# Optimization experiments

Measured on AMD Instinct MI355X. Metric: run time of the kernel, lower is better.

Reference implementation:

```python
import jax, jax.numpy as jnp
import numpy as np

N, D, F1, F2, F3, H = 4096, 512, 64, 32, 16, 4
ALPHA = 0.2  # LeakyReLU negative slope
NEG = -9e15


def setup_inputs() -> dict:
    key = jax.random.key(0)
    ks = jax.random.split(key, 11)
    # sparse binary adjacency with self loops (adj.to_dense() in original)
    adj = (jax.random.uniform(ks[1], (N, N)) < 0.01).astype(jnp.float32)
    adj = jnp.maximum(adj, jnp.eye(N, dtype=jnp.float32))
    return {
        "x": jax.random.normal(ks[0], (N, D), jnp.float32),
        "adj": adj,
        "W_heads": jax.random.normal(ks[2], (H, D, F1), jnp.float32) * 0.05,
        "a_heads": jax.random.normal(ks[3], (H, 2 * F1, 1), jnp.float32) * 0.05,
        "W_att": jax.random.normal(ks[4], (H * F1, F1), jnp.float32) * 0.05,
        "a_att": jax.random.normal(ks[5], (2 * F1, 1), jnp.float32) * 0.05,
        "W1": jax.random.normal(ks[6], (F1, F2), jnp.float32) * 0.05,
        "W2": jax.random.normal(ks[7], (F2, F3), jnp.float32) * 0.05,
        "W3": jax.random.normal(ks[8], (F2, F3), jnp.float32) * 0.05,
        "eps": jax.random.normal(ks[9], (N, F3), jnp.float32),
    }


def _gat(x, adj, W, a, out_dim):
    Wh = x @ W                                   # [N, F]
    e = (Wh @ a[:out_dim]) + (Wh @ a[out_dim:]).T  # [N,1] + [1,N] -> [N,N]
    e = jax.nn.leaky_relu(e, negative_slope=ALPHA)
    att = jax.nn.softmax(jnp.where(adj > 0, e, NEG), axis=-1)
    return jax.nn.elu(att @ Wh)                  # [N, F]


def reference(x, adj, W_heads, a_heads, W_att, a_att, W1, W2, W3, eps):
    # multi-head GAT, concat along feature dim
    heads = jax.vmap(lambda W, a: _gat(x, adj, W, a, F1))(W_heads, a_heads)  # [H,N,F1]
    cat = jnp.transpose(heads, (1, 0, 2)).reshape(N, H * F1)
    gc_att = _gat(cat, adj, W_att, a_att, F1)    # [N, F1]
    # GCN layers (dropout off, no bias): spmm(adj, x @ W)
    h1 = jax.nn.relu(adj @ (gc_att @ W1))        # [N, F2]
    mu = adj @ (h1 @ W2)                         # [N, F3]
    logvar = adj @ (h1 @ W3)                     # [N, F3]
    # reparameterize (vae_bool=True): eps * exp(logvar) + mu
    z = eps * jnp.exp(logvar) + mu
    adj_rec = z @ z.T                            # inner-product decoder [N,N]
    return adj_rec, mu, logvar
```

## Files before the change

kernel.cpp:

```cpp
#include <hip/hip_runtime.h>
#include <math.h>

#define NN 4096
#define DD 512
#define F1 64
#define F2 32
#define F3 16
#define NH 4
#define ALPHA 0.2f
#define CAP 160

__device__ __forceinline__ float lrelu(float e) { return (e >= 0.f) ? e : ALPHA * e; }

__global__ void k_csr(const float* __restrict__ adj, int* __restrict__ colidx,
                      int* __restrict__ deg) {
  __shared__ int cnt;
  int i = blockIdx.x, tid = threadIdx.x;
  if (tid == 0) cnt = 0;
  __syncthreads();
  const float4* arow = (const float4*)(adj + (size_t)i * NN);
  for (int t = tid; t < NN / 4; t += 256) {
    float4 v = arow[t];
    int base = t * 4;
    if (v.x != 0.f) { int p = atomicAdd(&cnt, 1); if (p < CAP) colidx[(size_t)i * CAP + p] = base; }
    if (v.y != 0.f) { int p = atomicAdd(&cnt, 1); if (p < CAP) colidx[(size_t)i * CAP + p] = base + 1; }
    if (v.z != 0.f) { int p = atomicAdd(&cnt, 1); if (p < CAP) colidx[(size_t)i * CAP + p] = base + 2; }
    if (v.w != 0.f) { int p = atomicAdd(&cnt, 1); if (p < CAP) colidx[(size_t)i * CAP + p] = base + 3; }
  }
  __syncthreads();
  if (tid == 0) deg[i] = cnt < CAP ? cnt : CAP;
}

__global__ __launch_bounds__(256) void k_wh_gemm(
    const float* __restrict__ x, const float* __restrict__ W_heads,
    const float* __restrict__ a_heads, float* __restrict__ Whcat,
    float* __restrict__ s1, float* __restrict__ s2) {
  __shared__ float As[2][32][65];
  __shared__ float Bs[2][32][64];
  int tid = threadIdx.x;
  int h = blockIdx.y;
  int r0 = blockIdx.x * 64;
  const float* Wh = W_heads + (size_t)h * DD * F1;

  int sr = tid >> 3, sq = tid & 7;
  int bk = tid >> 4, bf = tid & 15;
  int rg = tid >> 4, cg = tid & 15;

  const float* xa0 = x + (size_t)(r0 + sr) * DD;
  const float* xa1 = x + (size_t)(r0 + sr + 32) * DD;

  float4 pa0 = *(const float4*)(xa0 + sq * 4);
  float4 pa1 = *(const float4*)(xa1 + sq * 4);
  float4 pb0 = *(const float4*)(Wh + (size_t)bk * F1 + bf * 4);
  float4 pb1 = *(const float4*)(Wh + (size_t)(bk + 16) * F1 + bf * 4);
  {
    float* a0p = &As[0][sq * 4][sr];
    a0p[0] = pa0.x; a0p[65] = pa0.y; a0p[130] = pa0.z; a0p[195] = pa0.w;
    float* a1p = &As[0][sq * 4][sr + 32];
    a1p[0] = pa1.x; a1p[65] = pa1.y; a1p[130] = pa1.z; a1p[195] = pa1.w;
    *(float4*)&Bs[0][bk][bf * 4] = pb0;
    *(float4*)&Bs[0][bk + 16][bf * 4] = pb1;
  }
  __syncthreads();

  float acc[4][4] = {};
  for (int c = 0; c < 16; ++c) {
    int cb = c & 1;
    if (c < 15) {
      int k0 = (c + 1) * 32;
      pa0 = *(const float4*)(xa0 + k0 + sq * 4);
      pa1 = *(const float4*)(xa1 + k0 + sq * 4);
      pb0 = *(const float4*)(Wh + (size_t)(k0 + bk) * F1 + bf * 4);
      pb1 = *(const float4*)(Wh + (size_t)(k0 + bk + 16) * F1 + bf * 4);
    }
#pragma unroll
    for (int kk = 0; kk < 32; ++kk) {
      float4 av = *(const float4*)&As[cb][kk][rg * 4];
      float4 bv = *(const float4*)&Bs[cb][kk][cg * 4];
      acc[0][0] = fmaf(av.x, bv.x, acc[0][0]);
      acc[0][1] = fmaf(av.x, bv.y, acc[0][1]);
      acc[0][2] = fmaf(av.x, bv.z, acc[0][2]);
      acc[0][3] = fmaf(av.x, bv.w, acc[0][3]);
      acc[1][0] = fmaf(av.y, bv.x, acc[1][0]);
      acc[1][1] = fmaf(av.y, bv.y, acc[1][1]);
      acc[1][2] = fmaf(av.y, bv.z, acc[1][2]);
      acc[1][3] = fmaf(av.y, bv.w, acc[1][3]);
      acc[2][0] = fmaf(av.z, bv.x, acc[2][0]);
      acc[2][1] = fmaf(av.z, bv.y, acc[2][1]);
      acc[2][2] = fmaf(av.z, bv.z, acc[2][2]);
      acc[2][3] = fmaf(av.z, bv.w, acc[2][3]);
      acc[3][0] = fmaf(av.w, bv.x, acc[3][0]);
      acc[3][1] = fmaf(av.w, bv.y, acc[3][1]);
      acc[3][2] = fmaf(av.w, bv.z, acc[3][2]);
      acc[3][3] = fmaf(av.w, bv.w, acc[3][3]);
    }
    if (c < 15) {
      int nb = cb ^ 1;
      float* a0p = &As[nb][sq * 4][sr];
      a0p[0] = pa0.x; a0p[65] = pa0.y; a0p[130] = pa0.z; a0p[195] = pa0.w;
      float* a1p = &As[nb][sq * 4][sr + 32];
      a1p[0] = pa1.x; a1p[65] = pa1.y; a1p[130] = pa1.z; a1p[195] = pa1.w;
      *(float4*)&Bs[nb][bk][bf * 4] = pb0;
      *(float4*)&Bs[nb][bk + 16][bf * 4] = pb1;
      __syncthreads();
    }
  }

  float4 a1v = *(const float4*)&a_heads[h * 2 * F1 + cg * 4];
  float4 a2v = *(const float4*)&a_heads[h * 2 * F1 + F1 + cg * 4];
#pragma unroll
  for (int r = 0; r < 4; ++r) {
    int row = r0 + rg * 4 + r;
    *(float4*)&Whcat[(size_t)row * (NH * F1) + h * 64 + cg * 4] =
        make_float4(acc[r][0], acc[r][1], acc[r][2], acc[r][3]);
    float v1 = acc[r][0] * a1v.x + acc[r][1] * a1v.y + acc[r][2] * a1v.z + acc[r][3] * a1v.w;
    float v2 = acc[r][0] * a2v.x + acc[r][1] * a2v.y + acc[r][2] * a2v.z + acc[r][3] * a2v.w;
#pragma unroll
    for (int off = 8; off > 0; off >>= 1) {
      v1 += __shfl_down(v1, off, 16);
      v2 += __shfl_down(v2, off, 16);
    }
    if (cg == 0) {
      s1[h * NN + row] = v1;
      s2[h * NN + row] = v2;
    }
  }
}

__global__ void k_gat_heads(const int* __restrict__ colidx, const int* __restrict__ deg,
                            const float* __restrict__ Whcat,
                            const float* __restrict__ s1, const float* __restrict__ s2,
                            float* __restrict__ cat) {
  __shared__ int idx[CAP];
  __shared__ float wsh[NH][CAP];
  int i = blockIdx.x, tid = threadIdx.x;
  int c = deg[i];
  for (int t = tid; t < c; t += 256) idx[t] = colidx[(size_t)i * CAP + t];
  __syncthreads();
  int h = tid >> 6;
  int f = tid & 63;
  const float* s2h = s2 + h * NN;
  float s1v = s1[h * NN + i];
  float M = -INFINITY;
  for (int k = f; k < c; k += 64) {
    float v = s2h[idx[k]];
    wsh[h][k] = v;
    M = fmaxf(M, v);
  }
#pragma unroll
  for (int off = 32; off > 0; off >>= 1) M = fmaxf(M, __shfl_down(M, off, 64));
  M = __shfl(M, 0, 64);
  float m = lrelu(s1v + M);
  float lsum = 0.f;
  for (int k = f; k < c; k += 64) {
    float w = __expf(lrelu(s1v + wsh[h][k]) - m);
    wsh[h][k] = w;
    lsum += w;
  }
#pragma unroll
  for (int off = 32; off > 0; off >>= 1) lsum += __shfl_down(lsum, off, 64);
  float linv = 1.f / __shfl(lsum, 0, 64);
  __syncthreads();
  const float* base = Whcat + h * 64 + f;
  float a0 = 0.f, a1 = 0.f, a2 = 0.f, a3 = 0.f;
  int k = 0;
  for (; k + 4 <= c; k += 4) {
    int j0 = idx[k], j1 = idx[k + 1], j2 = idx[k + 2], j3 = idx[k + 3];
    a0 = fmaf(wsh[h][k],     base[(size_t)j0 * 256], a0);
    a1 = fmaf(wsh[h][k + 1], base[(size_t)j1 * 256], a1);
    a2 = fmaf(wsh[h][k + 2], base[(size_t)j2 * 256], a2);
    a3 = fmaf(wsh[h][k + 3], base[(size_t)j3 * 256], a3);
  }
  for (; k < c; ++k) a0 = fmaf(wsh[h][k], base[(size_t)idx[k] * 256], a0);
  float o = (a0 + a1 + a2 + a3) * linv;
  cat[(size_t)i * (NH * F1) + tid] = (o > 0.f) ? o : expm1f(o);
}

__global__ void k_wh2(const float* __restrict__ cat,
                      const float* __restrict__ W_att,
                      const float* __restrict__ a_att,
                      float* __restrict__ Wh2,
                      float* __restrict__ s1b, float* __restrict__ s2b) {
  const int ROWS = 8;
  __shared__ float cs[ROWS][NH * F1];
  int tid = threadIdx.x;
  int r0 = blockIdx.x * ROWS;
  const float4* csrc = (const float4*)(cat + (size_t)r0 * 256);
  for (int t = tid; t < ROWS * 256 / 4; t += 256) ((float4*)cs)[t] = csrc[t];
  __syncthreads();
  int g = tid >> 6;
  int f = tid & 63;
  float a1 = a_att[f], a2 = a_att[64 + f];
  const float* W = W_att + f;
#pragma unroll
  for (int rr = 0; rr < 2; ++rr) {
    int r = g * 2 + rr;
    float acc = 0.f;
    for (int k = 0; k < 256; k += 4) {
      float4 cv = *(const float4*)&cs[r][k];
      acc = fmaf(cv.x, W[(k + 0) * 64], acc);
      acc = fmaf(cv.y, W[(k + 1) * 64], acc);
      acc = fmaf(cv.z, W[(k + 2) * 64], acc);
      acc = fmaf(cv.w, W[(k + 3) * 64], acc);
    }
    Wh2[(size_t)(r0 + r) * 64 + f] = acc;
    float v1 = acc * a1, v2 = acc * a2;
#pragma unroll
    for (int off = 32; off > 0; off >>= 1) {
      v1 += __shfl_down(v1, off, 64);
      v2 += __shfl_down(v2, off, 64);
    }
    if (f == 0) { s1b[r0 + r] = v1; s2b[r0 + r] = v2; }
  }
}

__global__ void k_gat2t1(const int* __restrict__ colidx, const int* __restrict__ deg,
                         const float* __restrict__ Wh2,
                         const float* __restrict__ s1b, const float* __restrict__ s2b,
                         const float* __restrict__ W1, float* __restrict__ t1) {
  __shared__ int idx4[4][CAP];
  __shared__ float wsh4[4][CAP];
  __shared__ float grow[4][64];
  __shared__ float W1s[F1 * F2];
  int tid = threadIdx.x;
  int w = tid >> 6, f = tid & 63;
  int i = blockIdx.x * 4 + w;
  int c = deg[i];
  for (int t = tid; t < F1 * F2; t += 256) W1s[t] = W1[t];
  for (int k = f; k < c; k += 64) idx4[w][k] = colidx[(size_t)i * CAP + k];
  __syncthreads();
  float s1v = s1b[i];
  float M = -INFINITY;
  for (int k = f; k < c; k += 64) {
    float v = s2b[idx4[w][k]];
    wsh4[w][k] = v;
    M = fmaxf(M, v);
  }
#pragma unroll
  for (int off = 32; off > 0; off >>= 1) M = fmaxf(M, __shfl_down(M, off, 64));
  M = __shfl(M, 0, 64);
  float m = lrelu(s1v + M);
  float lsum = 0.f;
  for (int k = f; k < c; k += 64) {
    float wv = __expf(lrelu(s1v + wsh4[w][k]) - m);
    wsh4[w][k] = wv;
    lsum += wv;
  }
#pragma unroll
  for (int off = 32; off > 0; off >>= 1) lsum += __shfl_down(lsum, off, 64);
  float linv = 1.f / __shfl(lsum, 0, 64);
  __syncthreads();
  const float* base = Wh2 + f;
  float a0 = 0.f, a1 = 0.f, a2 = 0.f, a3 = 0.f;
  int k = 0;
  for (; k + 4 <= c; k += 4) {
    int j0 = idx4[w][k], j1 = idx4[w][k + 1], j2 = idx4[w][k + 2], j3 = idx4[w][k + 3];
    a0 = fmaf(wsh4[w][k],     base[(size_t)j0 * 64], a0);
    a1 = fmaf(wsh4[w][k + 1], base[(size_t)j1 * 64], a1);
    a2 = fmaf(wsh4[w][k + 2], base[(size_t)j2 * 64], a2);
    a3 = fmaf(wsh4[w][k + 3], base[(size_t)j3 * 64], a3);
  }
  for (; k < c; ++k) a0 = fmaf(wsh4[w][k], base[(size_t)idx4[w][k] * 64], a0);
  float o = (a0 + a1 + a2 + a3) * linv;
  grow[w][f] = (o > 0.f) ? o : expm1f(o);
  __syncthreads();
  if (f < F2) {
    float acc = 0.f;
#pragma unroll 8
    for (int kk = 0; kk < F1; ++kk) acc = fmaf(grow[w][kk], W1s[kk * F2 + f], acc);
    t1[(size_t)i * F2 + f] = acc;
  }
}

__global__ void k_gcn1t23(const int* __restrict__ colidx, const int* __restrict__ deg,
                          const float* __restrict__ t1,
                          const float* __restrict__ W2, const float* __restrict__ W3,
                          float* __restrict__ t23) {
  __shared__ int idx4[4][CAP];
  __shared__ float hrow[4][F2];
  __shared__ float Wc[F2 * 32];
  int tid = threadIdx.x;
  int w = tid >> 6, lane = tid & 63;
  int nb = lane >> 5, g = lane & 31;
  int i = blockIdx.x * 4 + w;
  int c = deg[i];
  for (int t = tid; t < F2 * 32; t += 256) {
    int kk = t >> 5, gg = t & 31;
    Wc[t] = (gg < 16) ? W2[kk * 16 + gg] : W3[kk * 16 + (gg - 16)];
  }
  for (int k = lane; k < c; k += 64) idx4[w][k] = colidx[(size_t)i * CAP + k];
  __syncthreads();
  float a0 = 0.f, a1 = 0.f;
  int k = nb;
  for (; k + 2 < c; k += 4) {
    a0 += t1[(size_t)idx4[w][k] * F2 + g];
    a1 += t1[(size_t)idx4[w][k + 2] * F2 + g];
  }
  for (; k < c; k += 2) a0 += t1[(size_t)idx4[w][k] * F2 + g];
  float tot = a0 + a1;
  tot += __shfl_xor(tot, 32, 64);
  float h1v = fmaxf(tot, 0.f);
  if (nb == 0) hrow[w][g] = h1v;
  __syncthreads();
  if (lane < 32) {
    float acc = 0.f;
#pragma unroll 8
    for (int kk = 0; kk < F2; ++kk) acc = fmaf(hrow[w][kk], Wc[kk * 32 + lane], acc);
    t23[(size_t)i * 32 + lane] = acc;
  }
}

__global__ void k_gcn2(const int* __restrict__ colidx, const int* __restrict__ deg,
                       const float* __restrict__ t23, const float* __restrict__ eps,
                       float* __restrict__ mu_out, float* __restrict__ lv_out,
                       float* __restrict__ z) {
  __shared__ int idx4[4][CAP];
  int tid = threadIdx.x;
  int w = tid >> 6, lane = tid & 63;
  int nb = lane >> 5, g = lane & 31;
  int i = blockIdx.x * 4 + w;
  int c = deg[i];
  for (int k = lane; k < c; k += 64) idx4[w][k] = colidx[(size_t)i * CAP + k];
  __syncthreads();
  float a0 = 0.f, a1 = 0.f;
  int k = nb;
  for (; k + 2 < c; k += 4) {
    a0 += t23[(size_t)idx4[w][k] * 32 + g];
    a1 += t23[(size_t)idx4[w][k + 2] * 32 + g];
  }
  for (; k < c; k += 2) a0 += t23[(size_t)idx4[w][k] * 32 + g];
  float tot = a0 + a1;
  tot += __shfl_xor(tot, 32, 64);
  float lvv = __shfl(tot, (lane & 31) + 16, 64);
  if (lane < 16) {
    mu_out[(size_t)i * 16 + g] = tot;
    z[(size_t)i * 16 + g] = eps[(size_t)i * 16 + g] * expf(lvv) + tot;
  } else if (lane < 32) {
    lv_out[(size_t)i * 16 + (g - 16)] = tot;
  }
}

__global__ void k_zzt(const float* __restrict__ z, float* __restrict__ out) {
  __shared__ float zr[64][17];
  __shared__ float zc[64][17];
  int bj = blockIdx.x, bi = blockIdx.y;
  int tid = threadIdx.x;
  for (int t = tid; t < 64 * 16; t += 256) {
    int r = t >> 4, kk = t & 15;
    zr[r][kk] = z[(size_t)(bi * 64 + r) * 16 + kk];
    zc[r][kk] = z[(size_t)(bj * 64 + r) * 16 + kk];
  }
  __syncthreads();
  int rg = tid >> 4;
  int cg = tid & 15;
  float acc[4][4] = {};
  for (int kk = 0; kk < 16; ++kk) {
    float av[4], bv[4];
#pragma unroll
    for (int t = 0; t < 4; ++t) av[t] = zr[rg * 4 + t][kk];
#pragma unroll
    for (int t = 0; t < 4; ++t) bv[t] = zc[cg * 4 + t][kk];
#pragma unroll
    for (int r = 0; r < 4; ++r)
#pragma unroll
      for (int cc = 0; cc < 4; ++cc) acc[r][cc] = fmaf(av[r], bv[cc], acc[r][cc]);
  }
#pragma unroll
  for (int r = 0; r < 4; ++r) {
    float4 v = make_float4(acc[r][0], acc[r][1], acc[r][2], acc[r][3]);
    *(float4*)&out[(size_t)(bi * 64 + rg * 4 + r) * NN + bj * 64 + cg * 4] = v;
  }
}

extern "C" void kernel_launch(void* const* d_in, const int* in_sizes, int n_in,
                              void* d_out, int out_size, void* d_ws, size_t ws_size,
                              hipStream_t stream) {
  const float* x       = (const float*)d_in[0];
  const float* adj     = (const float*)d_in[1];
  const float* W_heads = (const float*)d_in[2];
  const float* a_heads = (const float*)d_in[3];
  const float* W_att   = (const float*)d_in[4];
  const float* a_att   = (const float*)d_in[5];
  const float* W1      = (const float*)d_in[6];
  const float* W2      = (const float*)d_in[7];
  const float* W3      = (const float*)d_in[8];
  const float* eps     = (const float*)d_in[9];

  float* out = (float*)d_out;
  float* adj_rec = out;
  float* mu_out  = out + (size_t)NN * NN;
  float* lv_out  = mu_out + (size_t)NN * F3;

  float* ws = (float*)d_ws;
  float* Whcat = ws;               ws += (size_t)NN * NH * F1;
  float* s1    = ws;               ws += (size_t)NH * NN;
  float* s2    = ws;               ws += (size_t)NH * NN;
  float* cat   = ws;               ws += (size_t)NN * NH * F1;
  float* Wh2   = ws;               ws += (size_t)NN * F1;
  float* s1b   = ws;               ws += NN;
  float* s2b   = ws;               ws += NN;
  float* t1    = ws;               ws += (size_t)NN * F2;
  float* t23   = ws;               ws += (size_t)NN * 2 * F3;
  float* z     = ws;               ws += (size_t)NN * F3;
  int*   colidx = (int*)ws;        ws += (size_t)NN * CAP;
  int*   deg    = (int*)ws;        ws += NN;

  k_csr<<<NN, 256, 0, stream>>>(adj, colidx, deg);
  k_wh_gemm<<<dim3(64, 4), 256, 0, stream>>>(x, W_heads, a_heads, Whcat, s1, s2);
  k_gat_heads<<<NN, 256, 0, stream>>>(colidx, deg, Whcat, s1, s2, cat);
  k_wh2<<<NN / 8, 256, 0, stream>>>(cat, W_att, a_att, Wh2, s1b, s2b);
  k_gat2t1<<<NN / 4, 256, 0, stream>>>(colidx, deg, Wh2, s1b, s2b, W1, t1);
  k_gcn1t23<<<NN / 4, 256, 0, stream>>>(colidx, deg, t1, W2, W3, t23);
  k_gcn2<<<NN / 4, 256, 0, stream>>>(colidx, deg, t23, eps, mu_out, lv_out, z);
  k_zzt<<<dim3(64, 64), 256, 0, stream>>>(z, adj_rec);
}
```

Before: 224.6 us.

## Split-K the head projection GEMM with a separate reduction kernel

The x@W_heads GEMM originally launched only 256 blocks, each looping over all of K=512. It now splits K into 4 chunks across a third grid dimension, writing 4 partial results. A new combine kernel sums the partials and computes the attention score dot products s1/s2. This raises parallelism on a GPU with many CUs, at the cost of an extra launch and about 16MB of extra partial-buffer traffic.

```diff
diff --git a/kernel.cpp b/kernel.cpp
--- a/kernel.cpp
+++ b/kernel.cpp
@@ -9,6 +9,7 @@
 #define NH 4
 #define ALPHA 0.2f
 #define CAP 160
+#define KS 4
 
 __device__ __forceinline__ float lrelu(float e) { return (e >= 0.f) ? e : ALPHA * e; }
 
@@ -31,23 +32,23 @@
   if (tid == 0) deg[i] = cnt < CAP ? cnt : CAP;
 }
 
-__global__ __launch_bounds__(256) void k_wh_gemm(
+__global__ __launch_bounds__(256, 4) void k_wh_gemm(
     const float* __restrict__ x, const float* __restrict__ W_heads,
-    const float* __restrict__ a_heads, float* __restrict__ Whcat,
-    float* __restrict__ s1, float* __restrict__ s2) {
+    float* __restrict__ part) {
   __shared__ float As[2][32][65];
   __shared__ float Bs[2][32][64];
   int tid = threadIdx.x;
   int h = blockIdx.y;
   int r0 = blockIdx.x * 64;
-  const float* Wh = W_heads + (size_t)h * DD * F1;
+  int kq = blockIdx.z;
+  const float* Wh = W_heads + (size_t)h * DD * F1 + (size_t)kq * 128 * F1;
 
   int sr = tid >> 3, sq = tid & 7;
   int bk = tid >> 4, bf = tid & 15;
   int rg = tid >> 4, cg = tid & 15;
 
-  const float* xa0 = x + (size_t)(r0 + sr) * DD;
-  const float* xa1 = x + (size_t)(r0 + sr + 32) * DD;
+  const float* xa0 = x + (size_t)(r0 + sr) * DD + kq * 128;
+  const float* xa1 = x + (size_t)(r0 + sr + 32) * DD + kq * 128;
 
   float4 pa0 = *(const float4*)(xa0 + sq * 4);
   float4 pa1 = *(const float4*)(xa1 + sq * 4);
@@ -64,9 +65,9 @@
   __syncthreads();
 
   float acc[4][4] = {};
-  for (int c = 0; c < 16; ++c) {
+  for (int c = 0; c < 4; ++c) {
     int cb = c & 1;
-    if (c < 15) {
+    if (c < 3) {
       int k0 = (c + 1) * 32;
       pa0 = *(const float4*)(xa0 + k0 + sq * 4);
       pa1 = *(const float4*)(xa1 + k0 + sq * 4);
@@ -94,7 +95,7 @@
       acc[3][2] = fmaf(av.w, bv.z, acc[3][2]);
       acc[3][3] = fmaf(av.w, bv.w, acc[3][3]);
     }
-    if (c < 15) {
+    if (c < 3) {
       int nb = cb ^ 1;
       float* a0p = &As[nb][sq * 4][sr];
       a0p[0] = pa0.x; a0p[65] = pa0.y; a0p[130] = pa0.z; a0p[195] = pa0.w;
@@ -106,23 +107,40 @@
     }
   }
 
-  float4 a1v = *(const float4*)&a_heads[h * 2 * F1 + cg * 4];
-  float4 a2v = *(const float4*)&a_heads[h * 2 * F1 + F1 + cg * 4];
+  float* dst = part + (size_t)kq * NN * (NH * F1);
 #pragma unroll
   for (int r = 0; r < 4; ++r) {
     int row = r0 + rg * 4 + r;
-    *(float4*)&Whcat[(size_t)row * (NH * F1) + h * 64 + cg * 4] =
+    *(float4*)&dst[(size_t)row * (NH * F1) + h * 64 + cg * 4] =
         make_float4(acc[r][0], acc[r][1], acc[r][2], acc[r][3]);
-    float v1 = acc[r][0] * a1v.x + acc[r][1] * a1v.y + acc[r][2] * a1v.z + acc[r][3] * a1v.w;
-    float v2 = acc[r][0] * a2v.x + acc[r][1] * a2v.y + acc[r][2] * a2v.z + acc[r][3] * a2v.w;
-#pragma unroll
-    for (int off = 8; off > 0; off >>= 1) {
-      v1 += __shfl_down(v1, off, 16);
-      v2 += __shfl_down(v2, off, 16);
-    }
-    if (cg == 0) {
-      s1[h * NN + row] = v1;
-      s2[h * NN + row] = v2;
+  }
+}
+
+__global__ void k_wh_comb(const float* __restrict__ part,
+                          const float* __restrict__ a_heads,
+                          float* __restrict__ Whcat,
+                          float* __restrict__ s1, float* __restrict__ s2) {
+  int tid = threadIdx.x;
+  int r0 = blockIdx.x * 8;
+  int h = tid >> 6, f = tid & 63;
+  float a1 = a_heads[h * 2 * F1 + f];
+  float a2 = a_heads[h * 2 * F1 + F1 + f];
+  const size_t stride = (size_t)NN * (NH * F1);
+#pragma unroll
+  for (int r = 0; r < 8; ++r) {
+    size_t off = (size_t)(r0 + r) * (NH * F1) + tid;
+    float v = part[off] + part[off + stride] + part[off + 2 * stride] +
+              part[off + 3 * stride];
+    Whcat[off] = v;
+    float v1 = v * a1, v2 = v * a2;
+#pragma unroll
+    for (int o = 32; o > 0; o >>= 1) {
+      v1 += __shfl_down(v1, o, 64);
+      v2 += __shfl_down(v2, o, 64);
+    }
+    if (f == 0) {
+      s1[h * NN + r0 + r] = v1;
+      s2[h * NN + r0 + r] = v2;
     }
   }
 }
@@ -404,9 +422,11 @@
   float* z     = ws;               ws += (size_t)NN * F3;
   int*   colidx = (int*)ws;        ws += (size_t)NN * CAP;
   int*   deg    = (int*)ws;        ws += NN;
+  float* part  = (float*)ws;       ws += (size_t)KS * NN * NH * F1;
 
   k_csr<<<NN, 256, 0, stream>>>(adj, colidx, deg);
-  k_wh_gemm<<<dim3(64, 4), 256, 0, stream>>>(x, W_heads, a_heads, Whcat, s1, s2);
+  k_wh_gemm<<<dim3(64, NH, KS), 256, 0, stream>>>(x, W_heads, part);
+  k_wh_comb<<<NN / 8, 256, 0, stream>>>(part, a_heads, Whcat, s1, s2);
   k_gat_heads<<<NN, 256, 0, stream>>>(colidx, deg, Whcat, s1, s2, cat);
   k_wh2<<<NN / 8, 256, 0, stream>>>(cat, W_att, a_att, Wh2, s1b, s2b);
   k_gat2t1<<<NN / 4, 256, 0, stream>>>(colidx, deg, Wh2, s1b, s2b, W1, t1);
```

After: 229.1 us. 1.02x slower.
